# Kernel optimization log

Hardware: AMD Instinct MI355X
Metric: run time of the kernel (lower is better)

Reference implementation:

```python
import jax, jax.numpy as jnp
import numpy as np

HIDDEN = 2048
HEADS = 16
HEAD_DIM = HIDDEN // HEADS
BATCH = 2
SEQ = 2048
LN_EPS = 1e-5


def setup_inputs() -> dict:
    key = jax.random.key(0)
    ks = jax.random.split(key, 14)
    g = 0.02  # xavier gain used in _init_weights
    lim = g * np.sqrt(6.0 / (HIDDEN + HIDDEN))
    def lin_w(k):
        return jax.random.uniform(k, (HIDDEN, HIDDEN), jnp.float32, -lim, lim)
    inp = {
        "hidden_states": jax.random.normal(ks[0], (BATCH, SEQ, HIDDEN), jnp.float32),
        "cross_states": jax.random.normal(ks[1], (BATCH, SEQ, HIDDEN), jnp.float32),
        "Wq": lin_w(ks[2]), "bq": jnp.zeros((HIDDEN,), jnp.float32),
        "Wk": lin_w(ks[3]), "bk": jnp.zeros((HIDDEN,), jnp.float32),
        "Wv": lin_w(ks[4]), "bv": jnp.zeros((HIDDEN,), jnp.float32),
        "Wo": lin_w(ks[5]), "bo": jnp.zeros((HIDDEN,), jnp.float32),
        "Wg": jax.random.uniform(ks[6], (HIDDEN, HIDDEN), jnp.float32, -np.sqrt(6.0/(2*HIDDEN)), np.sqrt(6.0/(2*HIDDEN))),
        "bg": jnp.zeros((HIDDEN,), jnp.float32),
        "ln_gamma": jnp.ones((HIDDEN,), jnp.float32),
        "ln_beta": jnp.zeros((HIDDEN,), jnp.float32),
    }
    return inp


def reference(hidden_states, cross_states, Wq, bq, Wk, bk, Wv, bv, Wo, bo, Wg, bg, ln_gamma, ln_beta):
    B, S, H = hidden_states.shape
    scale = HEAD_DIM ** -0.5
    # projections (weights stored as [in, out]; equivalent to torch x @ W.T with W.T pre-applied)
    q = hidden_states @ Wq + bq
    k = cross_states @ Wk + bk
    v = cross_states @ Wv + bv
    # [B, S, H] -> [B, heads, S, head_dim]
    def split_heads(x):
        return x.reshape(B, -1, HEADS, HEAD_DIM).transpose(0, 2, 1, 3)
    q, k, v = split_heads(q), split_heads(k), split_heads(v)
    scores = jnp.einsum('bhqd,bhkd->bhqk', q, k) * scale
    probs = jax.nn.softmax(scores, axis=-1)
    attn = jnp.einsum('bhqk,bhkd->bhqd', probs, v)
    attn = attn.transpose(0, 2, 1, 3).reshape(B, -1, H)
    attn = attn @ Wo + bo
    gate = jax.nn.sigmoid(hidden_states @ Wg + bg)
    attn = gate * attn  # dropout rate 0 -> identity
    out = hidden_states + attn
    mu = jnp.mean(out, axis=-1, keepdims=True)
    var = jnp.mean(jnp.square(out - mu), axis=-1, keepdims=True)
    out = (out - mu) * jax.lax.rsqrt(var + LN_EPS) * ln_gamma + ln_beta
    return out
```

## Files before the change

### kernel.cpp

```cpp
#include <hip/hip_runtime.h>

typedef __bf16 bf16;
typedef bf16 bf16x8 __attribute__((ext_vector_type(8)));
typedef bf16 bf16x4 __attribute__((ext_vector_type(4)));
typedef float floatx4 __attribute__((ext_vector_type(4)));

#define HID 2048
#define MROWS 4096

__device__ __forceinline__ void gload_lds16(const bf16* g, bf16* l) {
    __builtin_amdgcn_global_load_lds((const __attribute__((address_space(1))) void*)g,
                                     (__attribute__((address_space(3))) void*)l, 16, 0, 0);
}

__global__ __launch_bounds__(256) void convert2_kernel(const float* __restrict__ X0, const float* __restrict__ X1,
                                                       bf16* __restrict__ Y0, bf16* __restrict__ Y1)
{
    const float* X = blockIdx.z ? X1 : X0;
    bf16* Y = blockIdx.z ? Y1 : Y0;
    const int i = (blockIdx.x * 256 + threadIdx.x) * 4;
    const float4 v = *(const float4*)(X + i);
    bf16x4 o;
    o[0] = (bf16)v.x; o[1] = (bf16)v.y; o[2] = (bf16)v.z; o[3] = (bf16)v.w;
    *(bf16x4*)(Y + i) = o;
}

__global__ __launch_bounds__(256) void transpose5_kernel(
    const float* __restrict__ W0, const float* __restrict__ W1, const float* __restrict__ W2,
    const float* __restrict__ W3, const float* __restrict__ W4,
    bf16* __restrict__ T0, bf16* __restrict__ T1, bf16* __restrict__ T2,
    bf16* __restrict__ T3, bf16* __restrict__ T4)
{
    const float* W; bf16* WT;
    switch (blockIdx.z) {
        case 0: W = W0; WT = T0; break;
        case 1: W = W1; WT = T1; break;
        case 2: W = W2; WT = T2; break;
        case 3: W = W3; WT = T3; break;
        default: W = W4; WT = T4; break;
    }
    __shared__ float tile[32][33];
    const int n0 = blockIdx.x * 32, k0 = blockIdx.y * 32;
    const int tx = threadIdx.x & 31, ty = threadIdx.x >> 5;
    #pragma unroll
    for (int r = 0; r < 32; r += 8)
        tile[ty + r][tx] = W[(size_t)(k0 + ty + r) * HID + n0 + tx];
    __syncthreads();
    #pragma unroll
    for (int r = 0; r < 32; r += 8)
        WT[(size_t)(n0 + ty + r) * HID + k0 + tx] = (bf16)tile[tx][ty + r];
}

__global__ __launch_bounds__(256) void transpose_v_kernel(const bf16* __restrict__ X, bf16* __restrict__ Y)
{
    __shared__ bf16 tile[32][33];
    const int b = blockIdx.z;
    const int c0 = blockIdx.x * 32, t0 = blockIdx.y * 32;
    const int tx = threadIdx.x & 31, ty = threadIdx.x >> 5;
    const bf16* Xb = X + (size_t)b * HID * HID;
    bf16* Yb = Y + (size_t)b * HID * HID;
    #pragma unroll
    for (int r = 0; r < 32; r += 8)
        tile[ty + r][tx] = Xb[(size_t)(t0 + ty + r) * HID + c0 + tx];
    __syncthreads();
    #pragma unroll
    for (int r = 0; r < 32; r += 8)
        Yb[(size_t)(c0 + ty + r) * HID + t0 + tx] = tile[tx][ty + r];
}

#define BAR() __builtin_amdgcn_s_barrier()
#define WAIT_VM(N) asm volatile("s_waitcnt vmcnt(" #N ")" ::: "memory")

#define READ_A(SLOT) do { \
    _Pragma("unroll") \
    for (int mf = 0; mf < 4; mf++) \
      _Pragma("unroll") \
      for (int ks = 0; ks < 2; ks++) \
        af[mf][ks] = *(const bf16x8*)((SLOT) + (wm + mf * 16 + l15) * 64 + (((ks * 4 + quad) ^ swz) * 8)); \
    } while (0)

#define READ_B(DST, SLOT) do { \
    _Pragma("unroll") \
    for (int nf = 0; nf < 2; nf++) \
      _Pragma("unroll") \
      for (int ks = 0; ks < 2; ks++) \
        DST[nf][ks] = *(const bf16x8*)((SLOT) + (wn + nf * 16 + l15) * 64 + (((ks * 4 + quad) ^ swz) * 8)); \
    } while (0)

#define STAGE_A(DSTSLOT, ROWOFF, KT) do { \
    gload_lds16(Asrc + (size_t)(ROWOFF) * HID + (KT),        (DSTSLOT) + ldsOff); \
    gload_lds16(Asrc + (size_t)((ROWOFF) + 64) * HID + (KT), (DSTSLOT) + ldsOff + 4096); } while (0)

#define STAGE_B(DSTSLOT, ROWOFF, KT) do { \
    gload_lds16(Bsrc + (size_t)(ROWOFF) * HID + (KT),        (DSTSLOT) + ldsOff); \
    gload_lds16(Bsrc + (size_t)((ROWOFF) + 64) * HID + (KT), (DSTSLOT) + ldsOff + 4096); } while (0)

#define MFMA_QUAD(BF, MH, NH) \
    __builtin_amdgcn_s_setprio(1); \
    _Pragma("unroll") \
    for (int ks = 0; ks < 2; ks++) \
      _Pragma("unroll") \
      for (int mf = 0; mf < 4; mf++) \
        _Pragma("unroll") \
        for (int nf = 0; nf < 2; nf++) \
          acc[(MH) * 4 + mf][(NH) * 2 + nf] = __builtin_amdgcn_mfma_f32_16x16x32_bf16( \
              af[mf][ks], BF[nf][ks], acc[(MH) * 4 + mf][(NH) * 2 + nf], 0, 0, 0); \
    __builtin_amdgcn_s_setprio(0);

__global__ __launch_bounds__(512, 2) void gemm_qgkv256_kernel(
    const bf16* __restrict__ H, const bf16* __restrict__ Cx,
    const bf16* __restrict__ Wqg, const bf16* __restrict__ Wkv,
    const float* __restrict__ bq, const float* __restrict__ bg,
    const float* __restrict__ bk, const float* __restrict__ bv,
    bf16* __restrict__ qo, bf16* __restrict__ go,
    bf16* __restrict__ ko, bf16* __restrict__ vo)
{
    constexpr int BK = 64;
    constexpr int NT = HID / BK;
    __shared__ __align__(16) bf16 Ar[4][128 * BK];
    __shared__ __align__(16) bf16 Br[4][128 * BK];
    const int z = blockIdx.z;
    const bf16* A  = z ? Cx : H;
    const bf16* BT = z ? Wkv : Wqg;
    const int tid = threadIdx.x;
    const int wave = tid >> 6, lane = tid & 63;
    const int m0 = blockIdx.x * 256, n0 = blockIdx.y * 256;
    const int wm = (wave & 1) * 64;
    const int wn = (wave >> 1) * 32;
    const int l15 = lane & 15, quad = lane >> 4;
    const int swz = l15 & 7;

    floatx4 acc[8][4] = {};

    const int hrow = tid >> 3;
    const int cc0  = (tid & 7) ^ (hrow & 7);
    const bf16* Asrc = A  + (size_t)(m0 + hrow) * HID + cc0 * 8;
    const bf16* Bsrc = BT + (size_t)(n0 + hrow) * HID + cc0 * 8;
    const int ldsOff = tid * 8;

    STAGE_A(Ar[0], 0,   0);
    STAGE_B(Br[0], 0,   0);
    STAGE_A(Ar[1], 128, 0);
    STAGE_B(Br[1], 128, 0);
    STAGE_A(Ar[2], 0,   BK);
    STAGE_B(Br[2], 0,   BK);
    WAIT_VM(4); BAR();

    bf16x8 af[4][2], bl[2][2], bh[2][2];
    READ_B(bl, Br[0]);

    for (int t = 0; t < NT; t++) {
        const int sw = (t & 1) << 1;
        bf16* a_lo   = Ar[sw];
        bf16* a_hi   = Ar[sw | 1];
        bf16* b_hi   = Br[sw | 1];
        bf16* a_hi_n = Ar[(sw | 1) ^ 2];
        bf16* b_hi_n = Br[(sw | 1) ^ 2];
        bf16* b_lo_n = Br[sw ^ 2];
        const int kt1 = (t + 1) * BK, kt2 = (t + 2) * BK;
        const bool g1 = (t + 1 < NT), g2 = (t + 2 < NT);

        READ_A(a_lo);
        if (g1) STAGE_A(a_hi_n, 128, kt1);
        MFMA_QUAD(bl, 0, 0);
        WAIT_VM(6); BAR();

        READ_B(bh, b_hi);
        if (g1) STAGE_B(b_hi_n, 128, kt1);
        MFMA_QUAD(bh, 0, 1);
        BAR();

        READ_A(a_hi);
        if (g2) STAGE_A(Ar[sw], 0, kt2);
        MFMA_QUAD(bl, 1, 0);
        WAIT_VM(6); BAR();

        if (g1) READ_B(bl, b_lo_n);
        if (g2) STAGE_B(Br[sw], 0, kt2);
        MFMA_QUAD(bh, 1, 1);
        BAR();
    }

    const bool half2 = (n0 >= HID);
    const float* bias = z ? (half2 ? bv : bk) : (half2 ? bg : bq);
    bf16* C = z ? (half2 ? vo : ko) : (half2 ? go : qo);
    const bool sig = (!z) && half2;
    const int nb = n0 - (half2 ? HID : 0);
    #pragma unroll
    for (int nh = 0; nh < 2; nh++)
    #pragma unroll
    for (int nf = 0; nf < 2; nf++) {
        const int col = nb + nh * 128 + wn + nf * 16 + l15;
        const float bvv = bias[col];
        #pragma unroll
        for (int mh = 0; mh < 2; mh++)
        #pragma unroll
        for (int mf = 0; mf < 4; mf++) {
            #pragma unroll
            for (int r = 0; r < 4; r++) {
                const int row = m0 + mh * 128 + wm + mf * 16 + quad * 4 + r;
                float val = acc[mh * 4 + mf][nh * 2 + nf][r] + bvv;
                if (sig) val = 1.0f / (1.0f + __expf(-val));
                C[(size_t)row * HID + col] = (bf16)val;
            }
        }
    }
}

__global__ __launch_bounds__(256) void gemm_bt_kernel(const bf16* __restrict__ A, const bf16* __restrict__ BT,
                                                      const float* __restrict__ bias, bf16* __restrict__ C)
{
    constexpr int BK = 64;
    __shared__ __align__(16) bf16 As[128 * BK];
    __shared__ __align__(16) bf16 Bs[128 * BK];
    const int tid = threadIdx.x;
    const int wave = tid >> 6, lane = tid & 63;
    const int m0 = blockIdx.x * 128, n0 = blockIdx.y * 128;
    const int wm = (wave & 1) * 64, wn = (wave >> 1) * 64;
    const int l15 = lane & 15, q = lane >> 4;
    const int swz = l15 & 7;
    floatx4 acc[4][4] = {};
    const int srow = tid >> 3;
    const int scc = ((tid & 7) ^ (srow & 7)) * 8;
    const bf16* Ag = A  + (size_t)(m0 + srow) * HID + scc;
    const bf16* Bg = BT + (size_t)(n0 + srow) * HID + scc;
    bf16* Asl = As + tid * 8;
    bf16* Bsl = Bs + tid * 8;

    for (int kt = 0; kt < HID; kt += BK) {
        __syncthreads();
        #pragma unroll
        for (int rr = 0; rr < 4; rr++) {
            gload_lds16(Ag + (size_t)(rr * 32) * HID + kt, Asl + rr * 2048);
            gload_lds16(Bg + (size_t)(rr * 32) * HID + kt, Bsl + rr * 2048);
        }
        __syncthreads();
        #pragma unroll
        for (int ks = 0; ks < 2; ks++) {
            const int cc = (ks * 4 + q) ^ swz;
            bf16x8 af[4], bfr[4];
            #pragma unroll
            for (int i = 0; i < 4; i++)
                af[i] = *(const bf16x8*)(As + (wm + i * 16 + l15) * 64 + cc * 8);
            #pragma unroll
            for (int j = 0; j < 4; j++)
                bfr[j] = *(const bf16x8*)(Bs + (wn + j * 16 + l15) * 64 + cc * 8);
            #pragma unroll
            for (int i = 0; i < 4; i++)
                #pragma unroll
                for (int j = 0; j < 4; j++)
                    acc[i][j] = __builtin_amdgcn_mfma_f32_16x16x32_bf16(af[i], bfr[j], acc[i][j], 0, 0, 0);
        }
    }
    #pragma unroll
    for (int j = 0; j < 4; j++) {
        const int col = n0 + wn + j * 16 + l15;
        const float bvv = bias[col];
        #pragma unroll
        for (int i = 0; i < 4; i++) {
            #pragma unroll
            for (int r = 0; r < 4; r++) {
                const int row = m0 + wm + i * 16 + q * 4 + r;
                C[(size_t)row * HID + col] = (bf16)(acc[i][j][r] + bvv);
            }
        }
    }
}

__global__ __launch_bounds__(256) void attention_mfma4_kernel(const bf16* __restrict__ Q, const bf16* __restrict__ K,
                                                              const bf16* __restrict__ Vt,
                                                              bf16* __restrict__ Op0, bf16* __restrict__ Op1,
                                                              float* __restrict__ lp0, float* __restrict__ lp1)
{
    constexpr int PP = 72;
    __shared__ __align__(16) bf16 Ks[64 * 128];
    __shared__ __align__(16) bf16 Vts[128 * 64];
    __shared__ __align__(16) bf16 Ps[128 * PP];

    const int tid = threadIdx.x;
    const int wave = tid >> 6, lane = tid & 63;
    const int l15 = lane & 15, quad = lane >> 4;
    const int swz = l15 & 7;
    const int b = blockIdx.x >> 4, h = blockIdx.x & 15;
    const int q0 = blockIdx.y * 128;
    const int kt0 = blockIdx.z * 1024;
    bf16* Op = blockIdx.z ? Op1 : Op0;
    float* lp = blockIdx.z ? lp1 : lp0;
    const bf16* Qg = Q + (size_t)(b * 2048) * HID + h * 128;
    const bf16* Kg = K + (size_t)b * 2048 * HID + h * 128;
    const bf16* Vg = Vt + (size_t)(b * 2048 + h * 128) * HID;

    const int wq0 = wave * 32;

    const float qsc = 0.08838834764831845f * 1.44269504f;
    bf16x8 qreg[2][4];
    #pragma unroll
    for (int s = 0; s < 2; s++)
        #pragma unroll
        for (int kk = 0; kk < 4; kk++) {
            bf16x8 t = *(const bf16x8*)(Qg + (size_t)(q0 + wq0 + s * 16 + l15) * HID + kk * 32 + quad * 8);
            #pragma unroll
            for (int e = 0; e < 8; e++) t[e] = (bf16)((float)t[e] * qsc);
            qreg[s][kk] = t;
        }

    const int krow = tid >> 4;
    const int kcc = ((tid & 15) ^ (krow & 7)) * 8;
    const bf16* KgS = Kg + (size_t)krow * HID + kcc;
    bf16* Ksl = Ks + tid * 8;
    const int vrow = tid >> 3;
    const int vcc = ((tid & 7) ^ (vrow & 7)) * 8;
    const bf16* VgS = Vg + (size_t)vrow * HID + vcc;
    bf16* Vsl = Vts + tid * 8;

    float lsum[2] = {0.f, 0.f};
    floatx4 oacc[2][8] = {};

    for (int kt = kt0; kt < kt0 + 1024; kt += 64) {
        __syncthreads();
        #pragma unroll
        for (int rr = 0; rr < 4; rr++)
            gload_lds16(KgS + (size_t)(kt + rr * 16) * HID, Ksl + rr * 2048);
        #pragma unroll
        for (int rr = 0; rr < 4; rr++)
            gload_lds16(VgS + (size_t)(rr * 32) * HID + kt, Vsl + rr * 2048);
        WAIT_VM(4);
        BAR();

        floatx4 sacc[4][2];
        #pragma unroll
        for (int j = 0; j < 4; j++)
            #pragma unroll
            for (int s = 0; s < 2; s++) sacc[j][s] = (floatx4){0.f, 0.f, 0.f, 0.f};
        __builtin_amdgcn_s_setprio(1);
        #pragma unroll
        for (int kk = 0; kk < 4; kk++) {
            const int cc = (kk * 4 + quad) ^ swz;
            #pragma unroll
            for (int j = 0; j < 4; j++) {
                const bf16x8 kf = *(const bf16x8*)(Ks + (j * 16 + l15) * 128 + cc * 8);
                #pragma unroll
                for (int s = 0; s < 2; s++)
                    sacc[j][s] = __builtin_amdgcn_mfma_f32_16x16x32_bf16(kf, qreg[s][kk], sacc[j][s], 0, 0, 0);
            }
        }
        __builtin_amdgcn_s_setprio(0);

        #pragma unroll
        for (int s = 0; s < 2; s++) {
            const int prow = wq0 + s * 16 + l15;
            float ps = 0.f;
            #pragma unroll
            for (int j = 0; j < 4; j++) {
                bf16x4 pw;
                #pragma unroll
                for (int r = 0; r < 4; r++) {
                    const float p = exp2f(sacc[j][s][r]);
                    ps += p;
                    pw[r] = (bf16)p;
                }
                *(bf16x4*)(Ps + prow * PP + j * 16 + quad * 4) = pw;
            }
            lsum[s] += ps;
        }

        WAIT_VM(0);
        BAR();

        __builtin_amdgcn_s_setprio(1);
        #pragma unroll
        for (int ks = 0; ks < 2; ks++) {
            const int cc = (ks * 4 + quad) ^ swz;
            bf16x8 pf[2];
            #pragma unroll
            for (int s = 0; s < 2; s++)
                pf[s] = *(const bf16x8*)(Ps + (wq0 + s * 16 + l15) * PP + ks * 32 + quad * 8);
            #pragma unroll
            for (int dt = 0; dt < 8; dt++) {
                const bf16x8 vf = *(const bf16x8*)(Vts + (dt * 16 + l15) * 64 + cc * 8);
                #pragma unroll
                for (int s = 0; s < 2; s++)
                    oacc[s][dt] = __builtin_amdgcn_mfma_f32_16x16x32_bf16(pf[s], vf, oacc[s][dt], 0, 0, 0);
            }
        }
        __builtin_amdgcn_s_setprio(0);
    }

    #pragma unroll
    for (int s = 0; s < 2; s++) {
        float l = lsum[s];
        l += __shfl_xor(l, 16);
        l += __shfl_xor(l, 32);
        if (quad == 0)
            lp[(size_t)(b * 2048 + q0 + wq0 + s * 16 + l15) * 16 + h] = l;
        #pragma unroll
        for (int r = 0; r < 4; r++) {
            const size_t row = (size_t)(b * 2048 + q0 + wq0 + s * 16 + quad * 4 + r);
            #pragma unroll
            for (int dt = 0; dt < 8; dt++)
                Op[row * HID + h * 128 + dt * 16 + l15] = (bf16)(oacc[s][dt][r]);
        }
    }
}

__global__ __launch_bounds__(256) void attn_combine_kernel(const bf16* __restrict__ O0, const bf16* __restrict__ O1,
                                                           const float* __restrict__ l0, const float* __restrict__ l1,
                                                           bf16* __restrict__ out)
{
    const int row = blockIdx.x;
    const int c0 = threadIdx.x * 8;
    const int h = c0 >> 7;
    const size_t base = (size_t)row * HID;
    const float inv = 1.f / (l0[row * 16 + h] + l1[row * 16 + h]);
    const bf16x8 a = *(const bf16x8*)(O0 + base + c0);
    const bf16x8 c = *(const bf16x8*)(O1 + base + c0);
    bf16x8 o;
    #pragma unroll
    for (int e = 0; e < 8; e++) o[e] = (bf16)(((float)a[e] + (float)c[e]) * inv);
    *(bf16x8*)(out + base + c0) = o;
}

__global__ __launch_bounds__(256) void ln_kernel(const float* __restrict__ hidden, const bf16* __restrict__ gate,
                                                 const bf16* __restrict__ attnp, const float* __restrict__ gamma,
                                                 const float* __restrict__ beta, float* __restrict__ out)
{
    __shared__ float red[4];
    __shared__ float red2[4];
    const int row = blockIdx.x;
    const int tid = threadIdx.x;
    const size_t base = (size_t)row * HID;
    const int c0 = tid * 8;
    const float4 h0 = *(const float4*)(hidden + base + c0);
    const float4 h1 = *(const float4*)(hidden + base + c0 + 4);
    const bf16x8 g = *(const bf16x8*)(gate + base + c0);
    const bf16x8 a = *(const bf16x8*)(attnp + base + c0);
    float t[8] = {h0.x, h0.y, h0.z, h0.w, h1.x, h1.y, h1.z, h1.w};
    float sum = 0.f;
    #pragma unroll
    for (int e = 0; e < 8; e++) { t[e] += (float)g[e] * (float)a[e]; sum += t[e]; }
    #pragma unroll
    for (int o = 1; o < 64; o <<= 1) sum += __shfl_xor(sum, o);
    const int wave = tid >> 6, lane = tid & 63;
    if (lane == 0) red[wave] = sum;
    __syncthreads();
    const float mu = (red[0] + red[1] + red[2] + red[3]) * (1.f / HID);
    float vs = 0.f;
    #pragma unroll
    for (int e = 0; e < 8; e++) { const float d = t[e] - mu; vs += d * d; }
    #pragma unroll
    for (int o = 1; o < 64; o <<= 1) vs += __shfl_xor(vs, o);
    if (lane == 0) red2[wave] = vs;
    __syncthreads();
    const float var = (red2[0] + red2[1] + red2[2] + red2[3]) * (1.f / HID);
    const float inv = rsqrtf(var + 1e-5f);
    float res[8];
    #pragma unroll
    for (int e = 0; e < 8; e++) res[e] = (t[e] - mu) * inv * gamma[c0 + e] + beta[c0 + e];
    *(float4*)(out + base + c0)     = make_float4(res[0], res[1], res[2], res[3]);
    *(float4*)(out + base + c0 + 4) = make_float4(res[4], res[5], res[6], res[7]);
}

extern "C" void kernel_launch(void* const* d_in, const int* in_sizes, int n_in,
                              void* d_out, int out_size, void* d_ws, size_t ws_size,
                              hipStream_t stream) {
    const float* hidden = (const float*)d_in[0];
    const float* cross  = (const float*)d_in[1];
    const float* Wq = (const float*)d_in[2];
    const float* bq = (const float*)d_in[3];
    const float* Wk = (const float*)d_in[4];
    const float* bk = (const float*)d_in[5];
    const float* Wv = (const float*)d_in[6];
    const float* bv = (const float*)d_in[7];
    const float* Wo = (const float*)d_in[8];
    const float* bo = (const float*)d_in[9];
    const float* Wg = (const float*)d_in[10];
    const float* bg = (const float*)d_in[11];
    const float* gamma = (const float*)d_in[12];
    const float* beta  = (const float*)d_in[13];
    float* out = (float*)d_out;

    char* ws = (char*)d_ws;
    const size_t MB = 1ull << 20;
    bf16* hbf  = (bf16*)(ws);
    bf16* cbf  = (bf16*)(ws + 16 * MB);
    bf16* WqgT = (bf16*)(ws + 32 * MB);
    bf16* WkvT = (bf16*)(ws + 48 * MB);
    bf16* WoT  = (bf16*)(ws + 64 * MB);
    bf16* qbf  = (bf16*)(ws + 72 * MB);
    bf16* kbf  = (bf16*)(ws + 88 * MB);
    bf16* vbf  = (bf16*)(ws + 104 * MB);
    bf16* gbf  = (bf16*)(ws + 120 * MB);
    bf16* abf  = (bf16*)(ws + 136 * MB);
    bf16* WgTp = WqgT + (size_t)HID * HID;
    bf16* WvTp = WkvT + (size_t)HID * HID;
    bf16* vtr  = cbf;
    bf16* Op0  = hbf;
    bf16* Op1  = WqgT;
    float* l0  = (float*)WkvT;
    float* l1  = (float*)((char*)WkvT + 1 * MB);
    bf16* pbf  = qbf;

    convert2_kernel<<<dim3(8192, 1, 2), 256, 0, stream>>>(hidden, cross, hbf, cbf);
    transpose5_kernel<<<dim3(64, 64, 5), 256, 0, stream>>>(Wq, Wg, Wk, Wv, Wo, WqgT, WgTp, WkvT, WvTp, WoT);
    gemm_qgkv256_kernel<<<dim3(16, 16, 2), 512, 0, stream>>>(hbf, cbf, WqgT, WkvT, bq, bg, bk, bv,
                                                             qbf, gbf, kbf, vbf);
    transpose_v_kernel<<<dim3(64, 64, 2), 256, 0, stream>>>(vbf, vtr);
    attention_mfma4_kernel<<<dim3(32, 16, 2), 256, 0, stream>>>(qbf, kbf, vtr, Op0, Op1, l0, l1);
    attn_combine_kernel<<<MROWS, 256, 0, stream>>>(Op0, Op1, l0, l1, abf);
    gemm_bt_kernel<<<dim3(32, 16), 256, 0, stream>>>(abf, WoT, bo, pbf);
    ln_kernel<<<MROWS, 256, 0, stream>>>(hidden, gbf, pbf, gamma, beta, out);
}
```

Before: 470.6 us.

## Drop split-K attention and combine kernel; normalize output inside attention

The attention kernel no longer splits the key dimension into two halves. Each block now walks all 2048 keys and divides by the row sum before writing bf16 output directly. This removes the attn_combine kernel and the extra partial-output and row-sum traffic through memory. In exchange the grid shrinks from 1024 to 512 blocks, each doing twice the serial work, which may lower occupancy and load balance across the GPU's compute units.

```diff
diff --git a/kernel.cpp b/kernel.cpp
--- a/kernel.cpp
+++ b/kernel.cpp
@@ -269,8 +269,7 @@
 
 __global__ __launch_bounds__(256) void attention_mfma4_kernel(const bf16* __restrict__ Q, const bf16* __restrict__ K,
                                                               const bf16* __restrict__ Vt,
-                                                              bf16* __restrict__ Op0, bf16* __restrict__ Op1,
-                                                              float* __restrict__ lp0, float* __restrict__ lp1)
+                                                              bf16* __restrict__ Op)
 {
     constexpr int PP = 72;
     __shared__ __align__(16) bf16 Ks[64 * 128];
@@ -283,9 +282,6 @@
     const int swz = l15 & 7;
     const int b = blockIdx.x >> 4, h = blockIdx.x & 15;
     const int q0 = blockIdx.y * 128;
-    const int kt0 = blockIdx.z * 1024;
-    bf16* Op = blockIdx.z ? Op1 : Op0;
-    float* lp = blockIdx.z ? lp1 : lp0;
     const bf16* Qg = Q + (size_t)(b * 2048) * HID + h * 128;
     const bf16* Kg = K + (size_t)b * 2048 * HID + h * 128;
     const bf16* Vg = Vt + (size_t)(b * 2048 + h * 128) * HID;
@@ -316,7 +312,7 @@
     float lsum[2] = {0.f, 0.f};
     floatx4 oacc[2][8] = {};
 
-    for (int kt = kt0; kt < kt0 + 1024; kt += 64) {
+    for (int kt = 0; kt < 2048; kt += 64) {
         __syncthreads();
         #pragma unroll
         for (int rr = 0; rr < 4; rr++)
@@ -391,33 +387,15 @@
         float l = lsum[s];
         l += __shfl_xor(l, 16);
         l += __shfl_xor(l, 32);
-        if (quad == 0)
-            lp[(size_t)(b * 2048 + q0 + wq0 + s * 16 + l15) * 16 + h] = l;
         #pragma unroll
         for (int r = 0; r < 4; r++) {
+            const float inv = 1.0f / __shfl(l, quad * 4 + r);
             const size_t row = (size_t)(b * 2048 + q0 + wq0 + s * 16 + quad * 4 + r);
             #pragma unroll
             for (int dt = 0; dt < 8; dt++)
-                Op[row * HID + h * 128 + dt * 16 + l15] = (bf16)(oacc[s][dt][r]);
-        }
-    }
-}
-
-__global__ __launch_bounds__(256) void attn_combine_kernel(const bf16* __restrict__ O0, const bf16* __restrict__ O1,
-                                                           const float* __restrict__ l0, const float* __restrict__ l1,
-                                                           bf16* __restrict__ out)
-{
-    const int row = blockIdx.x;
-    const int c0 = threadIdx.x * 8;
-    const int h = c0 >> 7;
-    const size_t base = (size_t)row * HID;
-    const float inv = 1.f / (l0[row * 16 + h] + l1[row * 16 + h]);
-    const bf16x8 a = *(const bf16x8*)(O0 + base + c0);
-    const bf16x8 c = *(const bf16x8*)(O1 + base + c0);
-    bf16x8 o;
-    #pragma unroll
-    for (int e = 0; e < 8; e++) o[e] = (bf16)(((float)a[e] + (float)c[e]) * inv);
-    *(bf16x8*)(out + base + c0) = o;
+                Op[row * HID + h * 128 + dt * 16 + l15] = (bf16)(oacc[s][dt][r] * inv);
+        }
+    }
 }
 
 __global__ __launch_bounds__(256) void ln_kernel(const float* __restrict__ hidden, const bf16* __restrict__ gate,
@@ -494,10 +472,6 @@
     bf16* WgTp = WqgT + (size_t)HID * HID;
     bf16* WvTp = WkvT + (size_t)HID * HID;
     bf16* vtr  = cbf;
-    bf16* Op0  = hbf;
-    bf16* Op1  = WqgT;
-    float* l0  = (float*)WkvT;
-    float* l1  = (float*)((char*)WkvT + 1 * MB);
     bf16* pbf  = qbf;
 
     convert2_kernel<<<dim3(8192, 1, 2), 256, 0, stream>>>(hidden, cross, hbf, cbf);
@@ -505,8 +479,7 @@
     gemm_qgkv256_kernel<<<dim3(16, 16, 2), 512, 0, stream>>>(hbf, cbf, WqgT, WkvT, bq, bg, bk, bv,
                                                              qbf, gbf, kbf, vbf);
     transpose_v_kernel<<<dim3(64, 64, 2), 256, 0, stream>>>(vbf, vtr);
-    attention_mfma4_kernel<<<dim3(32, 16, 2), 256, 0, stream>>>(qbf, kbf, vtr, Op0, Op1, l0, l1);
-    attn_combine_kernel<<<MROWS, 256, 0, stream>>>(Op0, Op1, l0, l1, abf);
+    attention_mfma4_kernel<<<dim3(32, 16), 256, 0, stream>>>(qbf, kbf, vtr, abf);
     gemm_bt_kernel<<<dim3(32, 16), 256, 0, stream>>>(abf, WoT, bo, pbf);
     ln_kernel<<<MROWS, 256, 0, stream>>>(hidden, gbf, pbf, gamma, beta, out);
 }
```

Result: no change. 469.0 us (-0.3%).
